# Performance work log

Measured on AMD Instinct MI355X. Metric: run time of the kernel, lower is better.

## Reference

```python
import jax, jax.numpy as jnp
import numpy as np

N_NODES = 100_000
N_EDGES = 1_600_000
N_TOKENS = 16
VOCAB = 32_000
TOK_DIM = 64
NODE_DIM = 64
HID = 128
FC = 128
NUM_GRAPHS = 1024


def setup_inputs() -> dict:
    key = jax.random.key(0)
    ks = jax.random.split(key, 14)
    emb = jax.random.normal(ks[0], (VOCAB, TOK_DIM), jnp.float32) * 0.02
    emb = emb.at[0].set(0.0)  # padding_idx=0 row is zero
    return {
        "x_token_idxs": jax.random.randint(ks[1], (N_NODES, N_TOKENS), 0, VOCAB),
        "edge_index": jax.random.randint(ks[2], (2, N_EDGES), 0, N_NODES),
        "batch": jnp.sort(jax.random.randint(ks[3], (N_NODES,), 0, NUM_GRAPHS)),
        "emb": emb,
        "Wp": jax.random.normal(ks[4], (TOK_DIM, NODE_DIM), jnp.float32) * (1.0 / np.sqrt(TOK_DIM)),
        "bp": jnp.zeros((NODE_DIM,), jnp.float32),
        "W1": jax.random.normal(ks[5], (NODE_DIM, HID), jnp.float32) * (1.0 / np.sqrt(NODE_DIM)),
        "b1": jnp.zeros((HID,), jnp.float32),
        "W2": jax.random.normal(ks[6], (HID, HID), jnp.float32) * (1.0 / np.sqrt(HID)),
        "b2": jnp.zeros((HID,), jnp.float32),
        "Wfc": jax.random.normal(ks[7], (HID, FC), jnp.float32) * (1.0 / np.sqrt(HID)),
        "bfc": jnp.zeros((FC,), jnp.float32),
        "Wout": jax.random.normal(ks[8], (FC, 1), jnp.float32) * (1.0 / np.sqrt(FC)),
        "bout": jnp.zeros((1,), jnp.float32),
    }


def reference(x_token_idxs, edge_index, batch, emb, Wp, bp, W1, b1, W2, b2, Wfc, bfc, Wout, bout):
    N = x_token_idxs.shape[0]
    # token embed -> mean pool over tokens -> node projection
    node = emb[x_token_idxs].mean(axis=1) @ Wp + bp  # [N, NODE_DIM]

    # GCN normalization with self-loops (PyG gcn_norm, symmetric)
    loops = jnp.arange(N)
    src = jnp.concatenate([edge_index[0], loops])
    dst = jnp.concatenate([edge_index[1], loops])
    deg = jax.ops.segment_sum(jnp.ones_like(dst, jnp.float32), dst, num_segments=N)
    dis = jnp.where(deg > 0, jax.lax.rsqrt(deg), 0.0)
    norm = (dis[src] * dis[dst])[:, None]  # [E+N, 1]

    def gcn(x, W, b):
        h = x @ W                                      # linear transform first (in->out)
        msg = h[src] * norm                            # gather + scale
        return jax.ops.segment_sum(msg, dst, num_segments=N) + b  # scatter-add + bias

    x = jax.nn.relu(gcn(node, W1, b1))
    x = jax.nn.relu(gcn(x, W2, b2))

    # global mean pool by graph id
    cnt = jax.ops.segment_sum(jnp.ones((N,), jnp.float32), batch, num_segments=NUM_GRAPHS)
    g = jax.ops.segment_sum(x, batch, num_segments=NUM_GRAPHS) / jnp.maximum(cnt, 1.0)[:, None]

    g = jax.nn.relu(g @ Wfc + bfc)
    logits = (g @ Wout + bout).squeeze(-1)  # [NUM_GRAPHS]
    return jax.nn.sigmoid(logits), logits
```

## Files before the change

kernel.cpp:

```cpp
#include <hip/hip_runtime.h>
#include <hip/hip_bf16.h>
#include <hip/hip_fp16.h>
#include <math.h>

#define N_TOKENS 16
#define TOK_DIM 64
#define NODE_DIM 64
#define HID 128
#define FC 128
#define NUM_GRAPHS 1024
#define NBUCK_MAX 512
#define CHUNK 8192

typedef _Float16 f16x8 __attribute__((ext_vector_type(8)));
typedef float f32x4 __attribute__((ext_vector_type(4)));

__device__ __forceinline__ __half2 shfl_xor_h2(__half2 v, int mask) {
    int i = *(int*)&v;
    i = __shfl_xor(i, mask);
    return *(__half2*)&i;
}

__global__ void prep_weights_kernel(const float* __restrict__ Wp, const float* __restrict__ W1,
                                    const float* __restrict__ W2, const float* __restrict__ bp,
                                    _Float16* __restrict__ Wf16t, _Float16* __restrict__ W2t,
                                    float* __restrict__ bf) {
    int n = blockIdx.x;
    int t = threadIdx.x;
    if (t < 64) {
        float acc = 0.f;
#pragma unroll
        for (int d = 0; d < 64; d++) acc += Wp[t * 64 + d] * W1[d * 128 + n];
        Wf16t[(size_t)n * 64 + t] = (_Float16)acc;
    } else {
        int d = t - 64;
        float v = bp[d] * W1[d * 128 + n];
#pragma unroll
        for (int off = 32; off > 0; off >>= 1) v += __shfl_down(v, off);
        if (d == 0) bf[n] = v;
    }
    W2t[(size_t)n * 128 + t] = (_Float16)W2[(size_t)t * 128 + n];
}

__global__ void convert_emb_kernel(const float* __restrict__ emb, __half* __restrict__ emb16,
                                   int n4) {
    int i = blockIdx.x * 256 + threadIdx.x;
    if (i < n4) {
        float4 v = ((const float4*)emb)[i];
        __half2 h0 = __floats2half2_rn(v.x, v.y);
        __half2 h1 = __floats2half2_rn(v.z, v.w);
        float2 p;
        ((__half2*)&p)[0] = h0;
        ((__half2*)&p)[1] = h1;
        ((float2*)emb16)[i] = p;
    }
}

__global__ void embed_mean_kernel(const int* __restrict__ tok,
                                  const __half* __restrict__ emb16,
                                  __half* __restrict__ mean16, int N) {
    int t = threadIdx.x;
    int w = t >> 6, j = t & 63;
    int q = j >> 3, l = j & 7;
    int i = blockIdx.x * 4 + w;
    if (i >= N) return;
    const float4* e4 = (const float4*)emb16;
    int t0 = tok[i * 16 + q];
    int t1 = tok[i * 16 + q + 8];
    float4 v0 = e4[(size_t)t0 * 8 + l];
    float4 v1 = e4[(size_t)t1 * 8 + l];
    const __half2* p0 = (const __half2*)&v0;
    const __half2* p1 = (const __half2*)&v1;
    __half2 a0 = __hadd2(p0[0], p1[0]);
    __half2 a1 = __hadd2(p0[1], p1[1]);
    __half2 a2 = __hadd2(p0[2], p1[2]);
    __half2 a3 = __hadd2(p0[3], p1[3]);
#pragma unroll
    for (int mask = 8; mask <= 32; mask <<= 1) {
        a0 = __hadd2(a0, shfl_xor_h2(a0, mask));
        a1 = __hadd2(a1, shfl_xor_h2(a1, mask));
        a2 = __hadd2(a2, shfl_xor_h2(a2, mask));
        a3 = __hadd2(a3, shfl_xor_h2(a3, mask));
    }
    if (q == 0) {
        __half2 inv = __floats2half2_rn(1.0f / 16.0f, 1.0f / 16.0f);
        float4 packed;
        __half2* pp = (__half2*)&packed;
        pp[0] = __hmul2(a0, inv);
        pp[1] = __hmul2(a1, inv);
        pp[2] = __hmul2(a2, inv);
        pp[3] = __hmul2(a3, inv);
        ((float4*)mean16)[(size_t)i * 8 + l] = packed;
    }
}

__global__ void bucket_hist_kernel(const int* __restrict__ dst, int* __restrict__ hist2d,
                                   int E, int nbuck) {
    __shared__ int h[NBUCK_MAX];
    int t = threadIdx.x;
    for (int i = t; i < nbuck; i += 512) h[i] = 0;
    __syncthreads();
    int base = blockIdx.x * CHUNK;
    for (int i = t; i < CHUNK; i += 512) {
        int e = base + i;
        if (e < E) atomicAdd(&h[dst[e] >> 8], 1);
    }
    __syncthreads();
    int* row = hist2d + (size_t)blockIdx.x * NBUCK_MAX;
    for (int i = t; i < nbuck; i += 512) row[i] = h[i];
}

__global__ void chunk_scan_kernel(const int* __restrict__ hist2d, int* __restrict__ chunkbase,
                                  int* __restrict__ total, int nchunk) {
    int b = blockIdx.x;
    int lane = threadIdx.x;
    int run = 0;
    for (int c0 = 0; c0 < nchunk; c0 += 64) {
        int c = c0 + lane;
        int v = (c < nchunk) ? hist2d[(size_t)c * NBUCK_MAX + b] : 0;
        int s = v;
#pragma unroll
        for (int off = 1; off < 64; off <<= 1) {
            int u = __shfl_up(s, off);
            if (lane >= off) s += u;
        }
        if (c < nchunk) chunkbase[(size_t)c * NBUCK_MAX + b] = s - v + run;
        run += __shfl(s, 63);
    }
    if (lane == 0) total[b] = run;
}

__global__ void bucket_scan_kernel(const int* __restrict__ total,
                                   int* __restrict__ bucket_base, int nbuck) {
    __shared__ int s[512];
    int tid = threadIdx.x;
    int v = (tid < nbuck) ? total[tid] : 0;
    s[tid] = v;
    __syncthreads();
    for (int off = 1; off < 512; off <<= 1) {
        int add = (tid >= off) ? s[tid - off] : 0;
        __syncthreads();
        s[tid] += add;
        __syncthreads();
    }
    if (tid < nbuck) bucket_base[tid] = s[tid] - v;
    if (tid == 511) bucket_base[nbuck] = s[511];
}

__global__ void binscatter_kernel(const int* __restrict__ src, const int* __restrict__ dst,
                                  const int* __restrict__ bucket_base,
                                  const int* __restrict__ chunkbase,
                                  int* __restrict__ staged, int E, int nbuck) {
    __shared__ int h[NBUCK_MAX];
    int t = threadIdx.x;
    const int* cb = chunkbase + (size_t)blockIdx.x * NBUCK_MAX;
    for (int i = t; i < nbuck; i += 512) h[i] = bucket_base[i] + cb[i];
    __syncthreads();
    int base = blockIdx.x * CHUNK;
    for (int i = t; i < CHUNK; i += 512) {
        int e = base + i;
        if (e < E) {
            int d = dst[e], s = src[e];
            int b = d >> 8;
            int r = atomicAdd(&h[b], 1);
            staged[r] = s | ((d & 255) << 17);
        }
    }
}

__global__ void bucket_count_kernel(const int* __restrict__ staged,
                                    const int* __restrict__ bucket_base,
                                    int* __restrict__ row_start, float* __restrict__ dis,
                                    int N, int E) {
    __shared__ int cnt[256];
    __shared__ int sc[256];
    int b = blockIdx.x;
    int t = threadIdx.x;
    cnt[t] = 0;
    __syncthreads();
    int rb0 = bucket_base[b], rb1 = bucket_base[b + 1];
    for (int i = rb0 + t; i < rb1; i += 256) atomicAdd(&cnt[staged[i] >> 17], 1);
    __syncthreads();
    int v = cnt[t];
    sc[t] = v;
    __syncthreads();
    for (int off = 1; off < 256; off <<= 1) {
        int add = (t >= off) ? sc[t - off] : 0;
        __syncthreads();
        sc[t] += add;
        __syncthreads();
    }
    int node = b * 256 + t;
    if (node < N) {
        row_start[node] = rb0 + sc[t] - v;
        dis[node] = rsqrtf(1.0f + (float)v);
    }
    if (b == 0 && t == 0) row_start[N] = E;
}

__global__ void csr_write_kernel(const int* __restrict__ staged,
                                 const int* __restrict__ bucket_base,
                                 const int* __restrict__ row_start,
                                 const float* __restrict__ dis,
                                 int2* __restrict__ csr, float* __restrict__ rowsum, int N) {
    __shared__ int cur[256];
    __shared__ float dl[256];
    __shared__ float wsum[256];
    int b = blockIdx.x;
    int t = threadIdx.x;
    int node = b * 256 + t;
    cur[t] = (node < N) ? row_start[node] : 0;
    dl[t] = (node < N) ? dis[node] : 0.f;
    wsum[t] = 0.f;
    __syncthreads();
    int rb0 = bucket_base[b], rb1 = bucket_base[b + 1];
    for (int i = rb0 + t; i < rb1; i += 256) {
        int v = staged[i];
        int s = v & 131071;
        int dloc = v >> 17;
        float w = dis[s] * dl[dloc];
        int pos = atomicAdd(&cur[dloc], 1);
        __half2 wh = __floats2half2_rn(w, w);
        csr[pos] = make_int2(s, *(int*)&wh);
        atomicAdd(&wsum[dloc], w);
    }
    __syncthreads();
    if (node < N) rowsum[node] = wsum[t] + dl[t] * dl[t];
}

__global__ __launch_bounds__(256, 8)
void agg64_kernel(const __half* __restrict__ mean16,
                  const int* __restrict__ row_start,
                  const int2* __restrict__ csr,
                  const float* __restrict__ dis,
                  __half* __restrict__ agg16, int N) {
    int t = threadIdx.x;
    int w = t >> 6, j = t & 63;
    int q = j >> 3, l = j & 7;
    int node = blockIdx.x * 4 + w;
    if (node >= N) return;
    int beg = row_start[node];
    int end = row_start[node + 1];
    float d = dis[node];
    const float4* m4 = (const float4*)mean16;
    __half2 a0, a1, a2, a3;
    {
        float4 raw = m4[(size_t)node * 8 + l];
        const __half2* hp = (const __half2*)&raw;
        float d2f = d * d * ((q == 0) ? 1.f : 0.f);
        __half2 d2h = __floats2half2_rn(d2f, d2f);
        a0 = __hmul2(hp[0], d2h); a1 = __hmul2(hp[1], d2h);
        a2 = __hmul2(hp[2], d2h); a3 = __hmul2(hp[3], d2h);
    }
    int k = beg;
    int kfull = beg + ((end - beg) & ~31);
    for (; k < kfull; k += 32) {
        int2 e[4];
        float4 v[4];
#pragma unroll
        for (int m = 0; m < 4; m++) e[m] = csr[k + 8 * m + q];
#pragma unroll
        for (int m = 0; m < 4; m++) v[m] = m4[(size_t)e[m].x * 8 + l];
#pragma unroll
        for (int m = 0; m < 4; m++) {
            __half2 wh = *(__half2*)&e[m].y;
            const __half2* hp = (const __half2*)&v[m];
            a0 = __hfma2(hp[0], wh, a0);
            a1 = __hfma2(hp[1], wh, a1);
            a2 = __hfma2(hp[2], wh, a2);
            a3 = __hfma2(hp[3], wh, a3);
        }
    }
    if (k < end) {
        int2 e[4];
        float4 v[4];
#pragma unroll
        for (int m = 0; m < 4; m++) {
            int kk = k + 8 * m + q;
            e[m] = (kk < end) ? csr[kk] : make_int2(0, 0);
        }
#pragma unroll
        for (int m = 0; m < 4; m++) v[m] = m4[(size_t)e[m].x * 8 + l];
#pragma unroll
        for (int m = 0; m < 4; m++) {
            __half2 wh = *(__half2*)&e[m].y;
            const __half2* hp = (const __half2*)&v[m];
            a0 = __hfma2(hp[0], wh, a0);
            a1 = __hfma2(hp[1], wh, a1);
            a2 = __hfma2(hp[2], wh, a2);
            a3 = __hfma2(hp[3], wh, a3);
        }
    }
#pragma unroll
    for (int mask = 8; mask <= 32; mask <<= 1) {
        a0 = __hadd2(a0, shfl_xor_h2(a0, mask));
        a1 = __hadd2(a1, shfl_xor_h2(a1, mask));
        a2 = __hadd2(a2, shfl_xor_h2(a2, mask));
        a3 = __hadd2(a3, shfl_xor_h2(a3, mask));
    }
    if (q == 0) {
        float4 packed;
        __half2* pp = (__half2*)&packed;
        pp[0] = a0; pp[1] = a1; pp[2] = a2; pp[3] = a3;
        ((float4*)agg16)[(size_t)node * 8 + l] = packed;
    }
}

#define NB 32
__global__ void dense_chain_mfma_kernel(const __half* __restrict__ agg16,
                                        const float* __restrict__ rowsum,
                                        const _Float16* __restrict__ Wf16t,
                                        const float* __restrict__ bf,
                                        const float* __restrict__ b1,
                                        const _Float16* __restrict__ W2t,
                                        __half* __restrict__ h2, int N) {
    __shared__ _Float16 sx1[32][136];
    __shared__ float srs[32];
    int t = threadIdx.x;
    int wv = t >> 6, lane = t & 63;
    int nb0 = blockIdx.x * NB;
    int rh = wv & 1;
    int ncb = (wv >> 1) * 64;
    int m16 = lane & 15;
    int q = lane >> 4;

    if (t < 32) srs[t] = (nb0 + t < N) ? rowsum[nb0 + t] : 0.f;

    f32x4 c0 = {}, c1 = {}, c2 = {}, c3 = {};
    int arow = nb0 + rh * 16 + m16;
    bool rowok = (arow < N);
    const _Float16* ag = (const _Float16*)agg16;
#pragma unroll
    for (int ks = 0; ks < 2; ks++) {
        int k0 = ks * 32 + q * 8;
        f16x8 afrag = {};
        if (rowok) afrag = *(const f16x8*)(ag + (size_t)arow * 64 + k0);
        f16x8 b0 = *(const f16x8*)(Wf16t + (size_t)(ncb + 0 * 16 + m16) * 64 + k0);
        f16x8 b1f = *(const f16x8*)(Wf16t + (size_t)(ncb + 1 * 16 + m16) * 64 + k0);
        f16x8 b2f = *(const f16x8*)(Wf16t + (size_t)(ncb + 2 * 16 + m16) * 64 + k0);
        f16x8 b3f = *(const f16x8*)(Wf16t + (size_t)(ncb + 3 * 16 + m16) * 64 + k0);
        c0 = __builtin_amdgcn_mfma_f32_16x16x32_f16(afrag, b0, c0, 0, 0, 0);
        c1 = __builtin_amdgcn_mfma_f32_16x16x32_f16(afrag, b1f, c1, 0, 0, 0);
        c2 = __builtin_amdgcn_mfma_f32_16x16x32_f16(afrag, b2f, c2, 0, 0, 0);
        c3 = __builtin_amdgcn_mfma_f32_16x16x32_f16(afrag, b3f, c3, 0, 0, 0);
    }
    __syncthreads();
    {
        f32x4 cc[4] = {c0, c1, c2, c3};
#pragma unroll
        for (int nt = 0; nt < 4; nt++) {
            int ncol = ncb + nt * 16 + m16;
            float bfj = bf[ncol], b1j = b1[ncol];
#pragma unroll
            for (int r = 0; r < 4; r++) {
                int mrow = q * 4 + r;
                float z = cc[nt][r] + srs[rh * 16 + mrow] * bfj + b1j;
                sx1[rh * 16 + mrow][ncol] = (_Float16)fmaxf(z, 0.f);
            }
        }
    }
    __syncthreads();

    f32x4 d0 = {}, d1 = {}, d2 = {}, d3 = {};
#pragma unroll
    for (int ks = 0; ks < 4; ks++) {
        int k0 = ks * 32 + q * 8;
        f16x8 afrag = *(const f16x8*)(&sx1[rh * 16 + m16][k0]);
        f16x8 b0 = *(const f16x8*)(W2t + (size_t)(ncb + 0 * 16 + m16) * 128 + k0);
        f16x8 b1f = *(const f16x8*)(W2t + (size_t)(ncb + 1 * 16 + m16) * 128 + k0);
        f16x8 b2f = *(const f16x8*)(W2t + (size_t)(ncb + 2 * 16 + m16) * 128 + k0);
        f16x8 b3f = *(const f16x8*)(W2t + (size_t)(ncb + 3 * 16 + m16) * 128 + k0);
        d0 = __builtin_amdgcn_mfma_f32_16x16x32_f16(afrag, b0, d0, 0, 0, 0);
        d1 = __builtin_amdgcn_mfma_f32_16x16x32_f16(afrag, b1f, d1, 0, 0, 0);
        d2 = __builtin_amdgcn_mfma_f32_16x16x32_f16(afrag, b2f, d2, 0, 0, 0);
        d3 = __builtin_amdgcn_mfma_f32_16x16x32_f16(afrag, b3f, d3, 0, 0, 0);
    }
    {
        f32x4 dd[4] = {d0, d1, d2, d3};
#pragma unroll
        for (int nt = 0; nt < 4; nt++) {
            int ncol = ncb + nt * 16 + m16;
#pragma unroll
            for (int r = 0; r < 4; r++) {
                int node = nb0 + rh * 16 + q * 4 + r;
                if (node < N) h2[(size_t)node * 128 + ncol] = __float2half(dd[nt][r]);
            }
        }
    }
}

__global__ __launch_bounds__(256, 8)
void gcn_agg128_kernel(const __half* __restrict__ hsrc,
                       const int* __restrict__ row_start,
                       const int2* __restrict__ csr,
                       const float* __restrict__ dis,
                       const float* __restrict__ b2,
                       __half* __restrict__ outx, int N) {
    int t = threadIdx.x;
    int w = t >> 6, j = t & 63;
    int q = j >> 4, l = j & 15;
    int node = blockIdx.x * 4 + w;
    if (node >= N) return;
    const float4* h4 = (const float4*)hsrc;
    int beg = row_start[node];
    int end = row_start[node + 1];
    float d = dis[node];
    __half2 a0, a1, a2, a3;
    {
        float4 raw = h4[(size_t)node * 16 + l];
        const __half2* hp = (const __half2*)&raw;
        float d2f = d * d * ((q == 0) ? 1.f : 0.f);
        __half2 d2h = __floats2half2_rn(d2f, d2f);
        a0 = __hmul2(hp[0], d2h); a1 = __hmul2(hp[1], d2h);
        a2 = __hmul2(hp[2], d2h); a3 = __hmul2(hp[3], d2h);
    }
    int k = beg;
    int kfull = beg + ((end - beg) & ~31);
    for (; k < kfull; k += 32) {
        int2 e[8];
        float4 v[8];
#pragma unroll
        for (int m = 0; m < 8; m++) e[m] = csr[k + 4 * m + q];
#pragma unroll
        for (int m = 0; m < 8; m++) v[m] = h4[(size_t)e[m].x * 16 + l];
#pragma unroll
        for (int m = 0; m < 8; m++) {
            __half2 wh = *(__half2*)&e[m].y;
            const __half2* hp = (const __half2*)&v[m];
            a0 = __hfma2(hp[0], wh, a0);
            a1 = __hfma2(hp[1], wh, a1);
            a2 = __hfma2(hp[2], wh, a2);
            a3 = __hfma2(hp[3], wh, a3);
        }
    }
    if (k < end) {
        int2 e[8];
        float4 v[8];
#pragma unroll
        for (int m = 0; m < 8; m++) {
            int kk = k + 4 * m + q;
            e[m] = (kk < end) ? csr[kk] : make_int2(0, 0);
        }
#pragma unroll
        for (int m = 0; m < 8; m++) v[m] = h4[(size_t)e[m].x * 16 + l];
#pragma unroll
        for (int m = 0; m < 8; m++) {
            __half2 wh = *(__half2*)&e[m].y;
            const __half2* hp = (const __half2*)&v[m];
            a0 = __hfma2(hp[0], wh, a0);
            a1 = __hfma2(hp[1], wh, a1);
            a2 = __hfma2(hp[2], wh, a2);
            a3 = __hfma2(hp[3], wh, a3);
        }
    }
#pragma unroll
    for (int mask = 16; mask <= 32; mask <<= 1) {
        a0 = __hadd2(a0, shfl_xor_h2(a0, mask));
        a1 = __hadd2(a1, shfl_xor_h2(a1, mask));
        a2 = __hadd2(a2, shfl_xor_h2(a2, mask));
        a3 = __hadd2(a3, shfl_xor_h2(a3, mask));
    }
    if (q == 0) {
        float2 f0 = __half22float2(a0), f1 = __half22float2(a1);
        float2 f2 = __half22float2(a2), f3 = __half22float2(a3);
        const float4* b4 = (const float4*)b2;
        float4 ba = b4[l * 2], bb = b4[l * 2 + 1];
        __half2 o0 = __floats2half2_rn(fmaxf(f0.x + ba.x, 0.f), fmaxf(f0.y + ba.y, 0.f));
        __half2 o1 = __floats2half2_rn(fmaxf(f1.x + ba.z, 0.f), fmaxf(f1.y + ba.w, 0.f));
        __half2 o2 = __floats2half2_rn(fmaxf(f2.x + bb.x, 0.f), fmaxf(f2.y + bb.y, 0.f));
        __half2 o3 = __floats2half2_rn(fmaxf(f3.x + bb.z, 0.f), fmaxf(f3.y + bb.w, 0.f));
        float4 packed;
        __half2* pp = (__half2*)&packed;
        pp[0] = o0; pp[1] = o1; pp[2] = o2; pp[3] = o3;
        ((float4*)outx)[(size_t)node * 16 + l] = packed;
    }
}

__device__ __forceinline__ int lower_bound_i(const int* __restrict__ a, int n, int val) {
    int lo = 0, hi = n;
    while (lo < hi) {
        int mid = (lo + hi) >> 1;
        if (a[mid] < val) lo = mid + 1; else hi = mid;
    }
    return lo;
}

__global__ void pool_head_kernel(const __half* __restrict__ x,
                                 const int* __restrict__ batch,
                                 const float* __restrict__ Wfc,
                                 const float* __restrict__ bfc,
                                 const float* __restrict__ Wout,
                                 const float* __restrict__ bout,
                                 float* __restrict__ out, int N) {
    int gr = blockIdx.x;
    int t = threadIdx.x;
    int j2 = t & 63, w = t >> 6;
    __shared__ float2 spart[4][64];
    __shared__ float sg[128];
    __shared__ float sfc[2][128];
    __shared__ float sred[128];
    int beg = lower_bound_i(batch, N, gr);
    int end = lower_bound_i(batch, N, gr + 1);
    const __half2* x2 = (const __half2*)x;
    float2 acc = make_float2(0.f, 0.f);
    for (int i = beg + w; i < end; i += 4) {
        float2 a = __half22float2(x2[(size_t)i * 64 + j2]);
        acc.x += a.x; acc.y += a.y;
    }
    spart[w][j2] = acc;
    __syncthreads();
    if (t < 64) {
        float inv = 1.0f / fmaxf((float)(end - beg), 1.0f);
        float2 s0 = spart[0][t], s1 = spart[1][t];
        float2 s2 = spart[2][t], s3 = spart[3][t];
        sg[2 * t] = (s0.x + s1.x + s2.x + s3.x) * inv;
        sg[2 * t + 1] = (s0.y + s1.y + s2.y + s3.y) * inv;
    }
    __syncthreads();
    int j = t & 127, hb = t >> 7;
    float a = 0.f;
#pragma unroll
    for (int k = 0; k < 64; k++) a += sg[hb * 64 + k] * Wfc[(hb * 64 + k) * 128 + j];
    sfc[hb][j] = a;
    __syncthreads();
    if (t < 128) {
        float aa = sfc[0][t] + sfc[1][t] + bfc[t];
        float f = fmaxf(aa, 0.f);
        sred[t] = f * Wout[t];
    }
    __syncthreads();
    if (t < 64) {
        float v = sred[t] + sred[t + 64];
#pragma unroll
        for (int off = 32; off > 0; off >>= 1) v += __shfl_down(v, off);
        if (t == 0) {
            float logit = v + bout[0];
            out[gr] = 1.0f / (1.0f + expf(-logit));
            out[NUM_GRAPHS + gr] = logit;
        }
    }
}

extern "C" void kernel_launch(void* const* d_in, const int* in_sizes, int n_in,
                              void* d_out, int out_size, void* d_ws, size_t ws_size,
                              hipStream_t stream) {
    const int* tok   = (const int*)d_in[0];
    const int* eidx  = (const int*)d_in[1];
    const int* batch = (const int*)d_in[2];
    const float* emb = (const float*)d_in[3];
    const float* Wp  = (const float*)d_in[4];
    const float* bp  = (const float*)d_in[5];
    const float* W1  = (const float*)d_in[6];
    const float* b1  = (const float*)d_in[7];
    const float* W2  = (const float*)d_in[8];
    const float* b2  = (const float*)d_in[9];
    const float* Wfc = (const float*)d_in[10];
    const float* bfc = (const float*)d_in[11];
    const float* Wout= (const float*)d_in[12];
    const float* bout= (const float*)d_in[13];
    float* out = (float*)d_out;

    const int N = in_sizes[2];
    const int E = in_sizes[1] / 2;
    const int* src = eidx;
    const int* dst = eidx + E;
    const int Np = (N + 3) & ~3;
    const int nbuck = (N + 255) / 256;
    const int nchunk = (E + CHUNK - 1) / CHUNK;
    const int emb_n4 = in_sizes[3] / 4;

    float* ws = (float*)d_ws;
    size_t off = 0;
    float* dis     = ws + off;            off += Np;
    __half* mean16 = (__half*)(ws + off); off += (size_t)Np * 32;
    __half* agg16  = (__half*)(ws + off); off += (size_t)Np * 32;
    float* rowsum  = ws + off;            off += Np;
    __half* h2buf  = (__half*)(ws + off); off += (size_t)Np * 64;
    __half* xfin16 = (__half*)(ws + off); off += (size_t)Np * 64;
    __half* emb16  = (__half*)(ws + off); off += (size_t)(in_sizes[3] / 2 + 4);
    _Float16* Wf16t = (_Float16*)(ws + off); off += 4096;
    _Float16* W2t   = (_Float16*)(ws + off); off += 8192;
    float* bf      = ws + off;            off += 128;
    int* row_start = (int*)(ws + off);    off += Np + 4;
    int* staged    = (int*)(ws + off);    off += E;
    int* total     = (int*)(ws + off);    off += NBUCK_MAX;
    int* bucket_base   = (int*)(ws + off); off += NBUCK_MAX + 8;
    int2* csr      = (int2*)(ws + off);
    int* hist2d    = (int*)h2buf;
    int* chunkbase = hist2d + (size_t)nchunk * NBUCK_MAX;

    prep_weights_kernel<<<128, 128, 0, stream>>>(Wp, W1, W2, bp, Wf16t, W2t, bf);
    convert_emb_kernel<<<(emb_n4 + 255) / 256, 256, 0, stream>>>(emb, emb16, emb_n4);

    bucket_hist_kernel<<<nchunk, 512, 0, stream>>>(dst, hist2d, E, nbuck);
    chunk_scan_kernel<<<nbuck, 64, 0, stream>>>(hist2d, chunkbase, total, nchunk);
    bucket_scan_kernel<<<1, 512, 0, stream>>>(total, bucket_base, nbuck);
    binscatter_kernel<<<nchunk, 512, 0, stream>>>(src, dst, bucket_base, chunkbase,
                                                  staged, E, nbuck);
    bucket_count_kernel<<<nbuck, 256, 0, stream>>>(staged, bucket_base, row_start, dis, N, E);
    csr_write_kernel<<<nbuck, 256, 0, stream>>>(staged, bucket_base, row_start, dis,
                                                csr, rowsum, N);

    embed_mean_kernel<<<(N + 3) / 4, 256, 0, stream>>>(tok, emb16, mean16, N);

    agg64_kernel<<<(N + 3) / 4, 256, 0, stream>>>(mean16, row_start, csr, dis, agg16, N);

    dense_chain_mfma_kernel<<<(N + NB - 1) / NB, 256, 0, stream>>>(agg16, rowsum, Wf16t,
                                                                   bf, b1, W2t, h2buf, N);

    gcn_agg128_kernel<<<(N + 3) / 4, 256, 0, stream>>>(h2buf, row_start, csr, dis, b2,
                                                       xfin16, N);

    pool_head_kernel<<<NUM_GRAPHS, 256, 0, stream>>>(xfin16, batch, Wfc, bfc, Wout, bout,
                                                     out, N);
}
```

Before: 329.1 us.

## Fuse 64-wide aggregation into dense MFMA chain and merge prep kernels

Merges the first-layer neighbor aggregation into the dense MFMA chain kernel. Each block of 4 waves aggregates 32 nodes, 8 per wave, into shared memory, then runs the two matrix multiplies from LDS. This removes the agg16 global round trip and one launch. Separately, the weight prep and embedding fp16 conversion kernels are folded into one launch. The catch is fewer parallel gather waves: 4 nodes per block become 32 nodes handled serially per wave, with occupancy lowered to 6 waves, which reduces latency hiding in the irregular gather.

```diff
diff --git a/kernel.cpp b/kernel.cpp
--- a/kernel.cpp
+++ b/kernel.cpp
@@ -21,38 +21,39 @@
     return *(__half2*)&i;
 }
 
-__global__ void prep_weights_kernel(const float* __restrict__ Wp, const float* __restrict__ W1,
-                                    const float* __restrict__ W2, const float* __restrict__ bp,
-                                    _Float16* __restrict__ Wf16t, _Float16* __restrict__ W2t,
-                                    float* __restrict__ bf) {
-    int n = blockIdx.x;
-    int t = threadIdx.x;
-    if (t < 64) {
-        float acc = 0.f;
-#pragma unroll
-        for (int d = 0; d < 64; d++) acc += Wp[t * 64 + d] * W1[d * 128 + n];
-        Wf16t[(size_t)n * 64 + t] = (_Float16)acc;
+__global__ void prep_fused_kernel(const float* __restrict__ Wp, const float* __restrict__ W1,
+                                  const float* __restrict__ W2, const float* __restrict__ bp,
+                                  const float* __restrict__ emb,
+                                  _Float16* __restrict__ Wf16t, _Float16* __restrict__ W2t,
+                                  float* __restrict__ bf, __half* __restrict__ emb16, int n4) {
+    int b = blockIdx.x;
+    int t = threadIdx.x;
+    if (b < 128) {
+        int n = b;
+        if (t < 64) {
+            float acc = 0.f;
+#pragma unroll
+            for (int d = 0; d < 64; d++) acc += Wp[t * 64 + d] * W1[d * 128 + n];
+            Wf16t[(size_t)n * 64 + t] = (_Float16)acc;
+        } else if (t < 128) {
+            int d = t - 64;
+            float v = bp[d] * W1[d * 128 + n];
+#pragma unroll
+            for (int off = 32; off > 0; off >>= 1) v += __shfl_down(v, off);
+            if (d == 0) bf[n] = v;
+        }
+        if (t < 128) W2t[(size_t)n * 128 + t] = (_Float16)W2[(size_t)t * 128 + n];
     } else {
-        int d = t - 64;
-        float v = bp[d] * W1[d * 128 + n];
-#pragma unroll
-        for (int off = 32; off > 0; off >>= 1) v += __shfl_down(v, off);
-        if (d == 0) bf[n] = v;
-    }
-    W2t[(size_t)n * 128 + t] = (_Float16)W2[(size_t)t * 128 + n];
-}
-
-__global__ void convert_emb_kernel(const float* __restrict__ emb, __half* __restrict__ emb16,
-                                   int n4) {
-    int i = blockIdx.x * 256 + threadIdx.x;
-    if (i < n4) {
-        float4 v = ((const float4*)emb)[i];
-        __half2 h0 = __floats2half2_rn(v.x, v.y);
-        __half2 h1 = __floats2half2_rn(v.z, v.w);
-        float2 p;
-        ((__half2*)&p)[0] = h0;
-        ((__half2*)&p)[1] = h1;
-        ((float2*)emb16)[i] = p;
+        int i = (b - 128) * 256 + t;
+        if (i < n4) {
+            float4 v = ((const float4*)emb)[i];
+            __half2 h0 = __floats2half2_rn(v.x, v.y);
+            __half2 h1 = __floats2half2_rn(v.z, v.w);
+            float2 p;
+            ((__half2*)&p)[0] = h0;
+            ((__half2*)&p)[1] = h1;
+            ((float2*)emb16)[i] = p;
+        }
     }
 }
 
@@ -228,113 +229,112 @@
     if (node < N) rowsum[node] = wsum[t] + dl[t] * dl[t];
 }
 
-__global__ __launch_bounds__(256, 8)
-void agg64_kernel(const __half* __restrict__ mean16,
-                  const int* __restrict__ row_start,
-                  const int2* __restrict__ csr,
-                  const float* __restrict__ dis,
-                  __half* __restrict__ agg16, int N) {
+#define NB 32
+__global__ __launch_bounds__(256, 6)
+void agg64_dense_kernel(const __half* __restrict__ mean16,
+                        const int* __restrict__ row_start,
+                        const int2* __restrict__ csr,
+                        const float* __restrict__ dis,
+                        const float* __restrict__ rowsum,
+                        const _Float16* __restrict__ Wf16t,
+                        const float* __restrict__ bf,
+                        const float* __restrict__ b1,
+                        const _Float16* __restrict__ W2t,
+                        __half* __restrict__ h2, int N) {
+    __shared__ _Float16 sagg[32][72];
+    __shared__ _Float16 sx1[32][136];
+    __shared__ float srs[32];
     int t = threadIdx.x;
     int w = t >> 6, j = t & 63;
     int q = j >> 3, l = j & 7;
-    int node = blockIdx.x * 4 + w;
-    if (node >= N) return;
-    int beg = row_start[node];
-    int end = row_start[node + 1];
-    float d = dis[node];
+    int nb0 = blockIdx.x * NB;
     const float4* m4 = (const float4*)mean16;
-    __half2 a0, a1, a2, a3;
-    {
-        float4 raw = m4[(size_t)node * 8 + l];
-        const __half2* hp = (const __half2*)&raw;
-        float d2f = d * d * ((q == 0) ? 1.f : 0.f);
-        __half2 d2h = __floats2half2_rn(d2f, d2f);
-        a0 = __hmul2(hp[0], d2h); a1 = __hmul2(hp[1], d2h);
-        a2 = __hmul2(hp[2], d2h); a3 = __hmul2(hp[3], d2h);
-    }
-    int k = beg;
-    int kfull = beg + ((end - beg) & ~31);
-    for (; k < kfull; k += 32) {
-        int2 e[4];
-        float4 v[4];
-#pragma unroll
-        for (int m = 0; m < 4; m++) e[m] = csr[k + 8 * m + q];
-#pragma unroll
-        for (int m = 0; m < 4; m++) v[m] = m4[(size_t)e[m].x * 8 + l];
-#pragma unroll
-        for (int m = 0; m < 4; m++) {
-            __half2 wh = *(__half2*)&e[m].y;
-            const __half2* hp = (const __half2*)&v[m];
-            a0 = __hfma2(hp[0], wh, a0);
-            a1 = __hfma2(hp[1], wh, a1);
-            a2 = __hfma2(hp[2], wh, a2);
-            a3 = __hfma2(hp[3], wh, a3);
-        }
-    }
-    if (k < end) {
-        int2 e[4];
-        float4 v[4];
-#pragma unroll
-        for (int m = 0; m < 4; m++) {
-            int kk = k + 8 * m + q;
-            e[m] = (kk < end) ? csr[kk] : make_int2(0, 0);
-        }
-#pragma unroll
-        for (int m = 0; m < 4; m++) v[m] = m4[(size_t)e[m].x * 8 + l];
-#pragma unroll
-        for (int m = 0; m < 4; m++) {
-            __half2 wh = *(__half2*)&e[m].y;
-            const __half2* hp = (const __half2*)&v[m];
-            a0 = __hfma2(hp[0], wh, a0);
-            a1 = __hfma2(hp[1], wh, a1);
-            a2 = __hfma2(hp[2], wh, a2);
-            a3 = __hfma2(hp[3], wh, a3);
-        }
-    }
-#pragma unroll
-    for (int mask = 8; mask <= 32; mask <<= 1) {
-        a0 = __hadd2(a0, shfl_xor_h2(a0, mask));
-        a1 = __hadd2(a1, shfl_xor_h2(a1, mask));
-        a2 = __hadd2(a2, shfl_xor_h2(a2, mask));
-        a3 = __hadd2(a3, shfl_xor_h2(a3, mask));
-    }
-    if (q == 0) {
-        float4 packed;
-        __half2* pp = (__half2*)&packed;
-        pp[0] = a0; pp[1] = a1; pp[2] = a2; pp[3] = a3;
-        ((float4*)agg16)[(size_t)node * 8 + l] = packed;
-    }
-}
-
-#define NB 32
-__global__ void dense_chain_mfma_kernel(const __half* __restrict__ agg16,
-                                        const float* __restrict__ rowsum,
-                                        const _Float16* __restrict__ Wf16t,
-                                        const float* __restrict__ bf,
-                                        const float* __restrict__ b1,
-                                        const _Float16* __restrict__ W2t,
-                                        __half* __restrict__ h2, int N) {
-    __shared__ _Float16 sx1[32][136];
-    __shared__ float srs[32];
-    int t = threadIdx.x;
-    int wv = t >> 6, lane = t & 63;
-    int nb0 = blockIdx.x * NB;
+
+    if (t < 32) srs[t] = (nb0 + t < N) ? rowsum[nb0 + t] : 0.f;
+
+    for (int s = 0; s < 8; s++) {
+        int node = nb0 + w * 8 + s;
+        __half2 a0, a1, a2, a3;
+        a0 = a1 = a2 = a3 = __floats2half2_rn(0.f, 0.f);
+        if (node < N) {
+            int beg = row_start[node];
+            int end = row_start[node + 1];
+            float d = dis[node];
+            {
+                float4 raw = m4[(size_t)node * 8 + l];
+                const __half2* hp = (const __half2*)&raw;
+                float d2f = d * d * ((q == 0) ? 1.f : 0.f);
+                __half2 d2h = __floats2half2_rn(d2f, d2f);
+                a0 = __hmul2(hp[0], d2h); a1 = __hmul2(hp[1], d2h);
+                a2 = __hmul2(hp[2], d2h); a3 = __hmul2(hp[3], d2h);
+            }
+            int k = beg;
+            int kfull = beg + ((end - beg) & ~31);
+            for (; k < kfull; k += 32) {
+                int2 e[4];
+                float4 v[4];
+#pragma unroll
+                for (int m = 0; m < 4; m++) e[m] = csr[k + 8 * m + q];
+#pragma unroll
+                for (int m = 0; m < 4; m++) v[m] = m4[(size_t)e[m].x * 8 + l];
+#pragma unroll
+                for (int m = 0; m < 4; m++) {
+                    __half2 wh = *(__half2*)&e[m].y;
+                    const __half2* hp = (const __half2*)&v[m];
+                    a0 = __hfma2(hp[0], wh, a0);
+                    a1 = __hfma2(hp[1], wh, a1);
+                    a2 = __hfma2(hp[2], wh, a2);
+                    a3 = __hfma2(hp[3], wh, a3);
+                }
+            }
+            if (k < end) {
+                int2 e[4];
+                float4 v[4];
+#pragma unroll
+                for (int m = 0; m < 4; m++) {
+                    int kk = k + 8 * m + q;
+                    e[m] = (kk < end) ? csr[kk] : make_int2(0, 0);
+                }
+#pragma unroll
+                for (int m = 0; m < 4; m++) v[m] = m4[(size_t)e[m].x * 8 + l];
+#pragma unroll
+                for (int m = 0; m < 4; m++) {
+                    __half2 wh = *(__half2*)&e[m].y;
+                    const __half2* hp = (const __half2*)&v[m];
+                    a0 = __hfma2(hp[0], wh, a0);
+                    a1 = __hfma2(hp[1], wh, a1);
+                    a2 = __hfma2(hp[2], wh, a2);
+                    a3 = __hfma2(hp[3], wh, a3);
+                }
+            }
+        }
+#pragma unroll
+        for (int mask = 8; mask <= 32; mask <<= 1) {
+            a0 = __hadd2(a0, shfl_xor_h2(a0, mask));
+            a1 = __hadd2(a1, shfl_xor_h2(a1, mask));
+            a2 = __hadd2(a2, shfl_xor_h2(a2, mask));
+            a3 = __hadd2(a3, shfl_xor_h2(a3, mask));
+        }
+        if (q == 0) {
+            float4 packed;
+            __half2* pp = (__half2*)&packed;
+            pp[0] = a0; pp[1] = a1; pp[2] = a2; pp[3] = a3;
+            *(float4*)(&sagg[w * 8 + s][l * 8]) = packed;
+        }
+    }
+    __syncthreads();
+
+    int wv = w, lane = j;
     int rh = wv & 1;
     int ncb = (wv >> 1) * 64;
     int m16 = lane & 15;
-    int q = lane >> 4;
-
-    if (t < 32) srs[t] = (nb0 + t < N) ? rowsum[nb0 + t] : 0.f;
+    int qq = lane >> 4;
 
     f32x4 c0 = {}, c1 = {}, c2 = {}, c3 = {};
-    int arow = nb0 + rh * 16 + m16;
-    bool rowok = (arow < N);
-    const _Float16* ag = (const _Float16*)agg16;
 #pragma unroll
     for (int ks = 0; ks < 2; ks++) {
-        int k0 = ks * 32 + q * 8;
-        f16x8 afrag = {};
-        if (rowok) afrag = *(const f16x8*)(ag + (size_t)arow * 64 + k0);
+        int k0 = ks * 32 + qq * 8;
+        f16x8 afrag = *(const f16x8*)(&sagg[rh * 16 + m16][k0]);
         f16x8 b0 = *(const f16x8*)(Wf16t + (size_t)(ncb + 0 * 16 + m16) * 64 + k0);
         f16x8 b1f = *(const f16x8*)(Wf16t + (size_t)(ncb + 1 * 16 + m16) * 64 + k0);
         f16x8 b2f = *(const f16x8*)(Wf16t + (size_t)(ncb + 2 * 16 + m16) * 64 + k0);
@@ -344,7 +344,6 @@
         c2 = __builtin_amdgcn_mfma_f32_16x16x32_f16(afrag, b2f, c2, 0, 0, 0);
         c3 = __builtin_amdgcn_mfma_f32_16x16x32_f16(afrag, b3f, c3, 0, 0, 0);
     }
-    __syncthreads();
     {
         f32x4 cc[4] = {c0, c1, c2, c3};
 #pragma unroll
@@ -353,7 +352,7 @@
             float bfj = bf[ncol], b1j = b1[ncol];
 #pragma unroll
             for (int r = 0; r < 4; r++) {
-                int mrow = q * 4 + r;
+                int mrow = qq * 4 + r;
                 float z = cc[nt][r] + srs[rh * 16 + mrow] * bfj + b1j;
                 sx1[rh * 16 + mrow][ncol] = (_Float16)fmaxf(z, 0.f);
             }
@@ -364,7 +363,7 @@
     f32x4 d0 = {}, d1 = {}, d2 = {}, d3 = {};
 #pragma unroll
     for (int ks = 0; ks < 4; ks++) {
-        int k0 = ks * 32 + q * 8;
+        int k0 = ks * 32 + qq * 8;
         f16x8 afrag = *(const f16x8*)(&sx1[rh * 16 + m16][k0]);
         f16x8 b0 = *(const f16x8*)(W2t + (size_t)(ncb + 0 * 16 + m16) * 128 + k0);
         f16x8 b1f = *(const f16x8*)(W2t + (size_t)(ncb + 1 * 16 + m16) * 128 + k0);
@@ -382,7 +381,7 @@
             int ncol = ncb + nt * 16 + m16;
 #pragma unroll
             for (int r = 0; r < 4; r++) {
-                int node = nb0 + rh * 16 + q * 4 + r;
+                int node = nb0 + rh * 16 + qq * 4 + r;
                 if (node < N) h2[(size_t)node * 128 + ncol] = __float2half(dd[nt][r]);
             }
         }
@@ -589,8 +588,8 @@
     int* hist2d    = (int*)h2buf;
     int* chunkbase = hist2d + (size_t)nchunk * NBUCK_MAX;
 
-    prep_weights_kernel<<<128, 128, 0, stream>>>(Wp, W1, W2, bp, Wf16t, W2t, bf);
-    convert_emb_kernel<<<(emb_n4 + 255) / 256, 256, 0, stream>>>(emb, emb16, emb_n4);
+    prep_fused_kernel<<<128 + (emb_n4 + 255) / 256, 256, 0, stream>>>(
+        Wp, W1, W2, bp, emb, Wf16t, W2t, bf, emb16, emb_n4);
 
     bucket_hist_kernel<<<nchunk, 512, 0, stream>>>(dst, hist2d, E, nbuck);
     chunk_scan_kernel<<<nbuck, 64, 0, stream>>>(hist2d, chunkbase, total, nchunk);
@@ -603,10 +602,9 @@
 
     embed_mean_kernel<<<(N + 3) / 4, 256, 0, stream>>>(tok, emb16, mean16, N);
 
-    agg64_kernel<<<(N + 3) / 4, 256, 0, stream>>>(mean16, row_start, csr, dis, agg16, N);
-
-    dense_chain_mfma_kernel<<<(N + NB - 1) / NB, 256, 0, stream>>>(agg16, rowsum, Wf16t,
-                                                                   bf, b1, W2t, h2buf, N);
+    agg64_dense_kernel<<<(N + NB - 1) / NB, 256, 0, stream>>>(mean16, row_start, csr, dis,
+                                                              rowsum, Wf16t, bf, b1, W2t,
+                                                              h2buf, N);
 
     gcn_agg128_kernel<<<(N + 3) / 4, 256, 0, stream>>>(h2buf, row_start, csr, dis, b2,
                                                        xfin16, N);
```

Result: faster. 317.0 us (-3.7%).
